# Optimization experiments

Measured on AMD Instinct MI355X. Metric: run time of the kernel, lower is better.

## Reference

```python
import jax, jax.numpy as jnp
import numpy as np

HIDDEN = 7168
N_HEADS = 32
QK_NOPE = 128
QK_ROPE = 64
V_DIM = 128
Q_LORA = 1536
KV_LORA = 512
ROPE_THETA = 10000.0
EPS = 1e-6
T = 2048
W_SCALE = 0.02


def setup_inputs() -> dict:
    key = jax.random.key(0)
    ks = jax.random.split(key, 8)
    return {
        "hidden_states": jax.random.normal(ks[0], (T, HIDDEN), jnp.float32),
        "positions": jnp.arange(T, dtype=jnp.int32),
        "wq_a": jax.random.normal(ks[1], (HIDDEN, Q_LORA), jnp.float32) * W_SCALE,
        "q_a_ln_w": jnp.ones((Q_LORA,), jnp.float32),
        "wq_b": jax.random.normal(ks[2], (Q_LORA, N_HEADS * (QK_NOPE + QK_ROPE)), jnp.float32) * W_SCALE,
        "wkv_a": jax.random.normal(ks[3], (HIDDEN, KV_LORA + QK_ROPE), jnp.float32) * W_SCALE,
        "kv_a_ln_w": jnp.ones((KV_LORA,), jnp.float32),
        "wkv_b": jax.random.normal(ks[4], (KV_LORA, N_HEADS * (QK_NOPE + V_DIM)), jnp.float32) * W_SCALE,
        "wo": jax.random.normal(ks[5], (N_HEADS * V_DIM, HIDDEN), jnp.float32) * W_SCALE,
    }


def _rmsnorm(x, w, eps=EPS):
    var = jnp.mean(jnp.square(x), axis=-1, keepdims=True)
    return x * jax.lax.rsqrt(var + eps) * w


def _rope_cos_sin(positions):
    # deepseek rope: base**(arange(0, d, 2)/d), interleaved (non-neox) layout
    inv_freq = 1.0 / (ROPE_THETA ** (jnp.arange(0, QK_ROPE, 2, dtype=jnp.float32) / QK_ROPE))
    ang = positions.astype(jnp.float32)[:, None] * inv_freq[None, :]  # [T, 32]
    return jnp.cos(ang), jnp.sin(ang)


def _apply_rope_interleaved(x, cos, sin):
    # x: [T, H, QK_ROPE]; even/odd interleaved pairs
    x1 = x[..., 0::2]
    x2 = x[..., 1::2]
    c = cos[:, None, :]
    s = sin[:, None, :]
    o1 = x1 * c - x2 * s
    o2 = x1 * s + x2 * c
    return jnp.stack([o1, o2], axis=-1).reshape(x.shape)


def reference(hidden_states, positions, wq_a, q_a_ln_w, wq_b, wkv_a, kv_a_ln_w, wkv_b, wo):
    scaling = (QK_NOPE + QK_ROPE) ** -0.5
    # q low-rank path: a-proj -> RMSNorm -> b-proj
    q = _rmsnorm(hidden_states @ wq_a, q_a_ln_w) @ wq_b  # [T, H*192]
    q = q.reshape(T, N_HEADS, QK_NOPE + QK_ROPE)
    q_nope, q_rope = q[..., :QK_NOPE], q[..., QK_NOPE:]
    # kv low-rank path
    latent = hidden_states @ wkv_a  # [T, KV_LORA + QK_ROPE]
    c_kv, k_rope = latent[:, :KV_LORA], latent[:, KV_LORA:]
    c_kv = _rmsnorm(c_kv, kv_a_ln_w)
    # decoupled RoPE on q_rope and shared k_rope
    cos, sin = _rope_cos_sin(positions)
    q_rope = _apply_rope_interleaved(q_rope, cos, sin)
    k_rope = _apply_rope_interleaved(k_rope[:, None, :], cos, sin)  # [T,1,64]
    # expand latent to per-head k_nope and v (kv_b_proj)
    kv = (c_kv @ wkv_b).reshape(T, N_HEADS, QK_NOPE + V_DIM)
    k_nope, v = kv[..., :QK_NOPE], kv[..., QK_NOPE:]
    k = jnp.concatenate([k_nope, jnp.broadcast_to(k_rope, (T, N_HEADS, QK_ROPE))], axis=-1)
    qf = jnp.concatenate([q_nope, q_rope], axis=-1)  # [T,H,192]
    # causal MHA
    scores = jnp.einsum("qhd,khd->hqk", qf, k) * scaling
    mask = jnp.tril(jnp.ones((T, T), dtype=bool))
    scores = jnp.where(mask[None], scores, -jnp.inf)
    p = jax.nn.softmax(scores, axis=-1)
    attn = jnp.einsum("hqk,khd->qhd", p, v).reshape(T, N_HEADS * V_DIM)
    return attn @ wo  # [T, HIDDEN]
```

## Files before the change

### kernel.cpp

```cpp
#include <hip/hip_runtime.h>
#include <stdint.h>

#define T_SEQ 2048
#define HID 7168
#define NH 32
#define DN 128
#define DR 64
#define DQK 192
#define DV 128
#define QL 1536
#define KVL 512
#define LATD 576
#define QD 6144
#define KVD 8192
#define WOK 4096
#define NCAT 2112

typedef unsigned short u16;
typedef __bf16 bf16x8 __attribute__((ext_vector_type(8)));
typedef float f32x4 __attribute__((ext_vector_type(4)));

__device__ __forceinline__ u16 f2bf(float f) {
  union { float f; unsigned u; } v; v.f = f;
  unsigned r = v.u + 0x7FFFu + ((v.u >> 16) & 1u);
  return (u16)(r >> 16);
}
__device__ __forceinline__ float bf2f(u16 s) {
  union { unsigned u; float f; } v; v.u = ((unsigned)s) << 16;
  return v.f;
}

__device__ __forceinline__ void gl2lds16(const void* g, void* l) {
  __builtin_amdgcn_global_load_lds((const __attribute__((address_space(1))) void*)g,
                                   (__attribute__((address_space(3))) void*)l, 16, 0, 0);
}

__device__ __forceinline__ f32x4 mfma16(bf16x8 a, bf16x8 b, f32x4 c) {
  return __builtin_amdgcn_mfma_f32_16x16x32_bf16(a, b, c, 0, 0, 0);
}

__device__ __forceinline__ void store_out(float* p, float v) { *p = v; }
__device__ __forceinline__ void store_out(u16* p, float v) { *p = f2bf(v); }

#define FENCE() asm volatile("" ::: "memory")

__global__ __launch_bounds__(256) void k_cvt_bf16(const float* __restrict__ in,
                                                  u16* __restrict__ out, long long n) {
  long long i = ((long long)blockIdx.x * 256 + threadIdx.x) * 8;
  if (i >= n) return;
  const float4* p = (const float4*)(in + i);
  float4 a = p[0], b = p[1];
  union { uint4 v; u16 s[8]; } o;
  o.s[0]=f2bf(a.x); o.s[1]=f2bf(a.y); o.s[2]=f2bf(a.z); o.s[3]=f2bf(a.w);
  o.s[4]=f2bf(b.x); o.s[5]=f2bf(b.y); o.s[6]=f2bf(b.z); o.s[7]=f2bf(b.w);
  *(uint4*)(out + i) = o.v;
}

__global__ __launch_bounds__(256) void k_transpose_bf16(const float* __restrict__ in,
                                                        u16* __restrict__ out, int R, int C,
                                                        float scale) {
  __shared__ float tile[64][65];
  int c0 = blockIdx.x * 64, r0 = blockIdx.y * 64;
  int tx = threadIdx.x & 15, ty = threadIdx.x >> 4;
  #pragma unroll
  for (int i = 0; i < 4; i++) {
    int r = ty + i * 16;
    float4 v = *(const float4*)(in + (size_t)(r0 + r) * C + c0 + tx * 4);
    tile[r][tx*4+0] = v.x; tile[r][tx*4+1] = v.y; tile[r][tx*4+2] = v.z; tile[r][tx*4+3] = v.w;
  }
  __syncthreads();
  #pragma unroll
  for (int i = 0; i < 4; i++) {
    int oc = ty + i * 16;
    union { uint2 v; u16 s[4]; } o;
    #pragma unroll
    for (int j = 0; j < 4; j++) o.s[j] = f2bf(tile[tx*4+j][oc] * scale);
    *(uint2*)(out + (size_t)(c0 + oc) * R + r0 + tx * 4) = o.v;
  }
}

__global__ __launch_bounds__(256) void k_rmsnorm_bf16(const float* __restrict__ x,
                                                      const float* __restrict__ w,
                                                      u16* __restrict__ out, int n, int ldin) {
  int row = blockIdx.x;
  const float* xr = x + (size_t)row * ldin;
  u16* orow = out + (size_t)row * n;
  float ss = 0.f;
  for (int i = threadIdx.x * 4; i < n; i += 1024) {
    float4 v = *(const float4*)(xr + i);
    ss += v.x*v.x + v.y*v.y + v.z*v.z + v.w*v.w;
  }
  #pragma unroll
  for (int off = 32; off > 0; off >>= 1) ss += __shfl_xor(ss, off);
  __shared__ float red[4];
  if ((threadIdx.x & 63) == 0) red[threadIdx.x >> 6] = ss;
  __syncthreads();
  float tot = red[0] + red[1] + red[2] + red[3];
  float rstd = rsqrtf(tot / (float)n + 1e-6f);
  for (int i = threadIdx.x * 4; i < n; i += 1024) {
    float4 v = *(const float4*)(xr + i);
    float4 g = *(const float4*)(w + i);
    union { uint2 u; u16 s[4]; } o;
    o.s[0]=f2bf(v.x*rstd*g.x); o.s[1]=f2bf(v.y*rstd*g.y);
    o.s[2]=f2bf(v.z*rstd*g.z); o.s[3]=f2bf(v.w*rstd*g.w);
    *(uint2*)(orow + i) = o.u;
  }
}

__global__ __launch_bounds__(256) void k_gemm_bt(const u16* __restrict__ A,
                                                 const u16* __restrict__ Bt,
                                                 float* __restrict__ C,
                                                 int M, int N, int K) {
  __shared__ __attribute__((aligned(16))) u16 As[128 * 32];
  __shared__ __attribute__((aligned(16))) u16 Bs[128 * 32];
  int m0 = blockIdx.y * 128, n0 = blockIdx.x * 128;
  int tid = threadIdx.x;
  int w = tid >> 6, lane = tid & 63, l16 = lane & 15, lh = lane >> 4;
  int wr = (w >> 1) * 64, wc = (w & 1) * 64;
  f32x4 zero = {0.f, 0.f, 0.f, 0.f};
  f32x4 acc[4][4];
  #pragma unroll
  for (int i = 0; i < 4; i++)
    #pragma unroll
    for (int j = 0; j < 4; j++) acc[i][j] = zero;
  int ra = tid >> 2, ca = (tid & 3) * 8;
  const u16* a0 = A + (size_t)(m0 + ra) * K + ca;
  const u16* a1 = A + (size_t)(m0 + ra + 64) * K + ca;
  int rb0 = n0 + ra;      rb0 = rb0 < N ? rb0 : N - 1;
  int rb1 = n0 + ra + 64; rb1 = rb1 < N ? rb1 : N - 1;
  const u16* b0 = Bt + (size_t)rb0 * K + ca;
  const u16* b1 = Bt + (size_t)rb1 * K + ca;
  for (int k0 = 0; k0 < K; k0 += 32) {
    gl2lds16(a0 + k0, &As[tid * 8]);
    gl2lds16(a1 + k0, &As[2048 + tid * 8]);
    gl2lds16(b0 + k0, &Bs[tid * 8]);
    gl2lds16(b1 + k0, &Bs[2048 + tid * 8]);
    __syncthreads();
    bf16x8 af[4], bv[4];
    #pragma unroll
    for (int i = 0; i < 4; i++) af[i] = *(const bf16x8*)&As[(wr + i * 16 + l16) * 32 + lh * 8];
    #pragma unroll
    for (int j = 0; j < 4; j++) bv[j] = *(const bf16x8*)&Bs[(wc + j * 16 + l16) * 32 + lh * 8];
    #pragma unroll
    for (int i = 0; i < 4; i++)
      #pragma unroll
      for (int j = 0; j < 4; j++)
        acc[i][j] = mfma16(af[i], bv[j], acc[i][j]);
    __syncthreads();
  }
  #pragma unroll
  for (int i = 0; i < 4; i++) {
    #pragma unroll
    for (int j = 0; j < 4; j++) {
      int col = n0 + wc + j * 16 + l16;
      if (col < N) {
        #pragma unroll
        for (int r = 0; r < 4; r++) {
          int row = m0 + wr + i * 16 + lh * 4 + r;
          C[(size_t)row * N + col] = acc[i][j][r];
        }
      }
    }
  }
}

template <typename OutT>
__global__ __launch_bounds__(512) void k_gemm_bt256(const u16* __restrict__ A,
                                                    const u16* __restrict__ Bt,
                                                    OutT* __restrict__ C,
                                                    int N, int K) {
  __shared__ __attribute__((aligned(16))) u16 lds[3 * 16384];
  const int tid = threadIdx.x;
  const int lane = tid & 63, l16 = lane & 15, lh = lane >> 4;
  const int w = tid >> 6, wm = w >> 2, wn = w & 3;
  const int m0 = blockIdx.y * 256, n0 = blockIdx.x * 256;
  const int nt = K >> 5;

  f32x4 acc[8][4];
  #pragma unroll
  for (int i = 0; i < 8; i++)
    #pragma unroll
    for (int j = 0; j < 4; j++) acc[i][j] = f32x4{0.f, 0.f, 0.f, 0.f};

  const int P = tid * 16;
  const int ls = P ^ (((P >> 7) & 7) << 4);
  const int sr = ls >> 6;
  const int sce = (ls & 63) >> 1;
  const u16* gA0 = A + (size_t)(m0 + sr) * K + sce;
  const u16* gA1 = A + (size_t)(m0 + sr + 128) * K + sce;
  const u16* gB0 = Bt + (size_t)(n0 + sr) * K + sce;
  const u16* gB1 = Bt + (size_t)(n0 + sr + 128) * K + sce;
  u16* ldst = &lds[tid * 8];

  for (int pt = 0; pt < 2 && pt < nt; ++pt) {
    gl2lds16(gA0 + pt * 32, ldst + pt * 16384);
    gl2lds16(gA1 + pt * 32, ldst + pt * 16384 + 4096);
    gl2lds16(gB0 + pt * 32, ldst + pt * 16384 + 8192);
    gl2lds16(gB1 + pt * 32, ldst + pt * 16384 + 12288);
  }
  __syncthreads();

  int bufr = 0;
  for (int t = 0; t < nt; ++t) {
    const bool more = (t + 2) < nt;
    const int bw = (t + 2) % 3;
    const u16* As = &lds[bufr * 16384];
    const u16* Bs = &lds[bufr * 16384 + 8192];
    bf16x8 afr[4], bfr[4];
    #pragma unroll
    for (int j = 0; j < 4; ++j) {
      int L = ((wn * 64 + j * 16 + l16) << 6) + (lh << 4);
      bfr[j] = *(const bf16x8*)((const char*)Bs + (L ^ (((L >> 7) & 7) << 4)));
    }
    #pragma unroll
    for (int i = 0; i < 4; ++i) {
      int L = ((wm * 128 + i * 16 + l16) << 6) + (lh << 4);
      afr[i] = *(const bf16x8*)((const char*)As + (L ^ (((L >> 7) & 7) << 4)));
    }
    if (more) {
      gl2lds16(gA0 + (t + 2) * 32, ldst + bw * 16384);
      gl2lds16(gA1 + (t + 2) * 32, ldst + bw * 16384 + 4096);
    }
    FENCE();
    __builtin_amdgcn_s_barrier();
    FENCE();
    __builtin_amdgcn_s_setprio(1);
    #pragma unroll
    for (int i = 0; i < 4; ++i)
      #pragma unroll
      for (int j = 0; j < 4; ++j)
        acc[i][j] = mfma16(afr[i], bfr[j], acc[i][j]);
    __builtin_amdgcn_s_setprio(0);
    FENCE();
    __builtin_amdgcn_s_barrier();
    FENCE();
    #pragma unroll
    for (int i = 0; i < 4; ++i) {
      int L = ((wm * 128 + 64 + i * 16 + l16) << 6) + (lh << 4);
      afr[i] = *(const bf16x8*)((const char*)As + (L ^ (((L >> 7) & 7) << 4)));
    }
    if (more) {
      gl2lds16(gB0 + (t + 2) * 32, ldst + bw * 16384 + 8192);
      gl2lds16(gB1 + (t + 2) * 32, ldst + bw * 16384 + 12288);
    }
    FENCE();
    __builtin_amdgcn_s_barrier();
    FENCE();
    __builtin_amdgcn_s_setprio(1);
    #pragma unroll
    for (int i = 0; i < 4; ++i)
      #pragma unroll
      for (int j = 0; j < 4; ++j)
        acc[4 + i][j] = mfma16(afr[i], bfr[j], acc[4 + i][j]);
    __builtin_amdgcn_s_setprio(0);
    FENCE();
    if (more) asm volatile("s_waitcnt vmcnt(4)" ::: "memory");
    else      asm volatile("s_waitcnt vmcnt(0)" ::: "memory");
    __builtin_amdgcn_s_barrier();
    FENCE();
    bufr = (bufr == 2) ? 0 : bufr + 1;
  }

  #pragma unroll
  for (int hf = 0; hf < 2; ++hf) {
    #pragma unroll
    for (int i = 0; i < 4; ++i) {
      int rbase = m0 + wm * 128 + hf * 64 + i * 16 + lh * 4;
      #pragma unroll
      for (int j = 0; j < 4; ++j) {
        int col = n0 + wn * 64 + j * 16 + l16;
        #pragma unroll
        for (int r = 0; r < 4; ++r)
          store_out(&C[(size_t)(rbase + r) * N + col], acc[hf * 4 + i][j][r]);
      }
    }
  }
}

__global__ __launch_bounds__(256) void k_build_q(const u16* __restrict__ qf,
                                                 const int* __restrict__ pos,
                                                 u16* __restrict__ Qc) {
  int t = blockIdx.x;
  __shared__ float cs[32], sn[32];
  if (threadIdx.x < 32) {
    float inv = expf(-9.2103403719761836f * (float)threadIdx.x / 32.f);
    float ang = (float)pos[t] * inv;
    cs[threadIdx.x] = cosf(ang);
    sn[threadIdx.x] = sinf(ang);
  }
  __syncthreads();
  const u16* qrow = qf + (size_t)t * QD;
  for (int e = threadIdx.x; e < QD; e += 256) {
    int h = e / 192, d = e - h * 192;
    u16 outv;
    if (d < DN) {
      outv = qrow[e];
    } else {
      int dr = d - DN, i = dr >> 1;
      float x1 = bf2f(qrow[h * 192 + DN + 2 * i]), x2 = bf2f(qrow[h * 192 + DN + 2 * i + 1]);
      float v = (dr & 1) ? (x1 * sn[i] + x2 * cs[i]) : (x1 * cs[i] - x2 * sn[i]);
      outv = f2bf(v);
    }
    Qc[((size_t)h * T_SEQ + t) * DQK + d] = outv;
  }
}

__global__ __launch_bounds__(256) void k_build_k(const u16* __restrict__ kvf,
                                                 const float* __restrict__ kr, int krld,
                                                 const int* __restrict__ pos,
                                                 u16* __restrict__ Kc) {
  int t = blockIdx.x;
  __shared__ u16 kro[64];
  if (threadIdx.x < 32) {
    int i = threadIdx.x;
    float inv = expf(-9.2103403719761836f * (float)i / 32.f);
    float ang = (float)pos[t] * inv;
    float c = cosf(ang), s = sinf(ang);
    float x1 = kr[(size_t)t * krld + 2 * i];
    float x2 = kr[(size_t)t * krld + 2 * i + 1];
    kro[2 * i]     = f2bf(x1 * c - x2 * s);
    kro[2 * i + 1] = f2bf(x1 * s + x2 * c);
  }
  __syncthreads();
  const u16* krow = kvf + (size_t)t * KVD;
  for (int e = threadIdx.x; e < NH * DQK; e += 256) {
    int h = e / 192, d = e - h * 192;
    Kc[((size_t)h * T_SEQ + t) * DQK + d] = (d < DN) ? krow[h * 256 + d] : kro[d - DN];
  }
}

__global__ __launch_bounds__(256) void k_build_vt(const u16* __restrict__ kvf,
                                                  u16* __restrict__ Vt) {
  __shared__ unsigned tile[64][65];
  int t0 = blockIdx.x * 64, d0 = blockIdx.y * 64, h = blockIdx.z;
  int tid = threadIdx.x;
  #pragma unroll
  for (int i = 0; i < 2; i++) {
    int r = (tid >> 3) + i * 32;
    int c = (tid & 7) * 8;
    uint4 v = *(const uint4*)(kvf + (size_t)(t0 + r) * KVD + h * 256 + DN + d0 + c);
    const u16* s = (const u16*)&v;
    #pragma unroll
    for (int j = 0; j < 8; j++) tile[r][c + j] = s[j];
  }
  __syncthreads();
  #pragma unroll
  for (int i = 0; i < 2; i++) {
    int d = (tid >> 3) + i * 32;
    int tb = (tid & 7) * 8;
    union { uint4 v; u16 s[8]; } o;
    #pragma unroll
    for (int j = 0; j < 8; j++) o.s[j] = (u16)tile[tb + j][d];
    *(uint4*)(Vt + ((size_t)h * DV + d0 + d) * T_SEQ + t0 + tb) = o.v;
  }
}

__global__ __launch_bounds__(256) void k_mla_attn(const u16* __restrict__ Qc,
                                                  const u16* __restrict__ Kc,
                                                  const u16* __restrict__ Vt,
                                                  u16* __restrict__ attn) {
  int qt = blockIdx.x, h = blockIdx.y;
  __shared__ __attribute__((aligned(16))) u16 Ks[64 * 192];
  __shared__ __attribute__((aligned(16))) u16 Vs[128 * 64];
  __shared__ __attribute__((aligned(16))) u16 Ps[64 * 64];
  int tid = threadIdx.x, w = tid >> 6, lane = tid & 63, l16 = lane & 15, lh = lane >> 4;
  int swz = (l16 & 7) << 4;

  const char* Qg = (const char*)(Qc + ((size_t)h * T_SEQ + (size_t)qt * 64) * DQK);
  #pragma unroll
  for (int i = 0; i < 6; i++) {
    int L = tid * 16 + i * 4096;
    int row = L / 384;
    gl2lds16(Qg + (L ^ ((row & 7) << 4)), (char*)Ks + L);
  }
  __syncthreads();
  bf16x8 aq[6];
  #pragma unroll
  for (int kf = 0; kf < 6; kf++)
    aq[kf] = *(const bf16x8*)((const char*)Ks + (w * 16 + l16) * 384 + ((kf * 64 + lh * 16) ^ swz));
  __syncthreads();

  f32x4 zero = {0.f, 0.f, 0.f, 0.f};
  f32x4 accO[8];
  #pragma unroll
  for (int i = 0; i < 8; i++) accO[i] = zero;
  float m[4]    = {-3e38f, -3e38f, -3e38f, -3e38f};
  float lsum[4] = {0.f, 0.f, 0.f, 0.f};

  const char* Kb = (const char*)(Kc + (size_t)h * T_SEQ * DQK);
  const char* Vb = (const char*)(Vt + (size_t)h * DV * T_SEQ);

  for (int kt = 0; kt <= qt; ++kt) {
    const char* Kg = Kb + (size_t)kt * 64 * DQK * 2;
    #pragma unroll
    for (int i = 0; i < 6; i++) {
      int L = tid * 16 + i * 4096;
      int row = L / 384;
      gl2lds16(Kg + (L ^ ((row & 7) << 4)), (char*)Ks + L);
    }
    #pragma unroll
    for (int i = 0; i < 4; i++) {
      int L = tid * 16 + i * 4096;
      int row = L >> 7, wb = L & 127;
      gl2lds16(Vb + (size_t)row * (T_SEQ * 2) + (size_t)kt * 128 + (wb ^ ((row & 7) << 4)),
               (char*)Vs + L);
    }
    __syncthreads();

    f32x4 sf[4];
    #pragma unroll
    for (int j = 0; j < 4; j++) sf[j] = zero;
    #pragma unroll
    for (int kf = 0; kf < 6; ++kf) {
      #pragma unroll
      for (int j = 0; j < 4; ++j) {
        bf16x8 bk = *(const bf16x8*)((const char*)Ks + (j * 16 + l16) * 384 +
                                     ((kf * 64 + lh * 16) ^ swz));
        sf[j] = mfma16(aq[kf], bk, sf[j]);
      }
    }
    bool diag = (kt == qt);
    #pragma unroll
    for (int rr = 0; rr < 4; ++rr) {
      int qrow = qt * 64 + w * 16 + lh * 4 + rr;
      float rowm = -3e38f;
      #pragma unroll
      for (int j = 0; j < 4; ++j) {
        float s = sf[j][rr];
        if (diag && (kt * 64 + j * 16 + l16) > qrow) s = -3e38f;
        sf[j][rr] = s;
        rowm = fmaxf(rowm, s);
      }
      rowm = fmaxf(rowm, __shfl_xor(rowm, 1));
      rowm = fmaxf(rowm, __shfl_xor(rowm, 2));
      rowm = fmaxf(rowm, __shfl_xor(rowm, 4));
      rowm = fmaxf(rowm, __shfl_xor(rowm, 8));
      float mnew = fmaxf(m[rr], rowm);
      float sc = __expf(m[rr] - mnew);
      float pj[4];
      float ps = 0.f;
      #pragma unroll
      for (int j = 0; j < 4; ++j) { pj[j] = __expf(sf[j][rr] - mnew); ps += pj[j]; }
      ps += __shfl_xor(ps, 1); ps += __shfl_xor(ps, 2);
      ps += __shfl_xor(ps, 4); ps += __shfl_xor(ps, 8);
      lsum[rr] = lsum[rr] * sc + ps;
      m[rr] = mnew;
      #pragma unroll
      for (int of = 0; of < 8; ++of) accO[of][rr] *= sc;
      int r = w * 16 + lh * 4 + rr;
      int rsw = (r & 7) << 4;
      #pragma unroll
      for (int j = 0; j < 4; ++j)
        *(u16*)((char*)Ps + r * 128 + ((2 * (j * 16 + l16)) ^ rsw)) = f2bf(pj[j]);
    }
    #pragma unroll
    for (int kf = 0; kf < 2; ++kf) {
      bf16x8 ap = *(const bf16x8*)((const char*)Ps + (w * 16 + l16) * 128 +
                                   ((kf * 64 + lh * 16) ^ swz));
      #pragma unroll
      for (int of = 0; of < 8; ++of) {
        bf16x8 bvv = *(const bf16x8*)((const char*)Vs + (of * 16 + l16) * 128 +
                                      ((kf * 64 + lh * 16) ^ swz));
        accO[of] = mfma16(ap, bvv, accO[of]);
      }
    }
    __syncthreads();
  }
  #pragma unroll
  for (int rr = 0; rr < 4; ++rr) {
    float inv = 1.f / lsum[rr];
    int t = qt * 64 + w * 16 + lh * 4 + rr;
    #pragma unroll
    for (int of = 0; of < 8; ++of)
      attn[(size_t)t * WOK + h * DV + of * 16 + l16] = f2bf(accO[of][rr] * inv);
  }
}

extern "C" void kernel_launch(void* const* d_in, const int* in_sizes, int n_in,
                              void* d_out, int out_size, void* d_ws, size_t ws_size,
                              hipStream_t stream) {
  const float* hidden     = (const float*)d_in[0];
  const int*   positions  = (const int*)d_in[1];
  const float* wq_a       = (const float*)d_in[2];
  const float* q_a_ln_w   = (const float*)d_in[3];
  const float* wq_b       = (const float*)d_in[4];
  const float* wkv_a      = (const float*)d_in[5];
  const float* kv_a_ln_w  = (const float*)d_in[6];
  const float* wkv_b      = (const float*)d_in[7];
  const float* wo         = (const float*)d_in[8];
  float* out = (float*)d_out;

  char* p = (char*)d_ws;
  size_t off = 0;
  auto alloc = [&](size_t bytes) -> void* {
    void* r = p + off;
    off += (bytes + 255) & ~(size_t)255;
    return r;
  };
  u16*   h_bf = (u16*)  alloc((size_t)T_SEQ * HID * 2);
  u16*   wbuf = (u16*)  alloc((size_t)HID * WOK * 2);
  u16*   bigh = (u16*)  alloc((size_t)T_SEQ * KVD * 2);
  float* cat  = (float*)alloc((size_t)T_SEQ * NCAT * 4);
  u16*   qln  = (u16*)  alloc((size_t)T_SEQ * QL * 2);
  u16*   ckv  = (u16*)  alloc((size_t)T_SEQ * KVL * 2);
  u16*   Qc   = (u16*)  alloc((size_t)NH * T_SEQ * DQK * 2);
  u16*   Kc   = (u16*)  alloc((size_t)NH * T_SEQ * DQK * 2);
  u16*   Vt   = (u16*)  alloc((size_t)NH * DV * T_SEQ * 2);
  u16*   attn = (u16*)  alloc((size_t)T_SEQ * WOK * 2);

  k_cvt_bf16<<<(T_SEQ * HID) / (256 * 8), 256, 0, stream>>>(hidden, h_bf, (long long)T_SEQ * HID);

  k_transpose_bf16<<<dim3(QL / 64, HID / 64), 256, 0, stream>>>(wq_a, wbuf, HID, QL, 1.0f);
  k_transpose_bf16<<<dim3(LATD / 64, HID / 64), 256, 0, stream>>>(wkv_a, wbuf + (size_t)QL * HID,
                                                                  HID, LATD, 1.0f);
  k_gemm_bt<<<dim3((NCAT + 127) / 128, T_SEQ / 128), 256, 0, stream>>>(h_bf, wbuf, cat,
                                                                       T_SEQ, NCAT, HID);

  k_rmsnorm_bf16<<<T_SEQ, 256, 0, stream>>>(cat + QL, kv_a_ln_w, ckv, KVL, NCAT);
  k_transpose_bf16<<<dim3(KVD / 64, KVL / 64), 256, 0, stream>>>(wkv_b, wbuf, KVL, KVD, 1.0f);
  k_gemm_bt256<u16><<<dim3(KVD / 256, T_SEQ / 256), 512, 0, stream>>>(ckv, wbuf, bigh, KVD, KVL);
  k_build_k<<<T_SEQ, 256, 0, stream>>>(bigh, cat + QL + KVL, NCAT, positions, Kc);
  k_build_vt<<<dim3(T_SEQ / 64, 2, NH), 256, 0, stream>>>(bigh, Vt);

  k_rmsnorm_bf16<<<T_SEQ, 256, 0, stream>>>(cat, q_a_ln_w, qln, QL, NCAT);
  k_transpose_bf16<<<dim3(QD / 64, QL / 64), 256, 0, stream>>>(wq_b, wbuf, QL, QD,
                                                               0.07216878364870322f);
  k_gemm_bt256<u16><<<dim3(QD / 256, T_SEQ / 256), 512, 0, stream>>>(qln, wbuf, bigh, QD, QL);
  k_build_q<<<T_SEQ, 256, 0, stream>>>(bigh, positions, Qc);

  k_mla_attn<<<dim3(T_SEQ / 64, NH), 256, 0, stream>>>(Qc, Kc, Vt, attn);

  k_transpose_bf16<<<dim3(HID / 64, WOK / 64), 256, 0, stream>>>(wo, wbuf, WOK, HID, 1.0f);
  k_gemm_bt256<float><<<dim3(HID / 256, T_SEQ / 256), 512, 0, stream>>>(attn, wbuf, out, HID, WOK);
}
```

Before: 676.1 us.

## Double-buffer K tiles, read V into registers, schedule heaviest query tiles first

The attention kernel now prefetches the next K tile into a second LDS buffer while the current tile is being computed, instead of loading and then waiting at a barrier. V fragments are loaded straight from global memory into registers for each tile, so the V shared-memory buffer is gone. The grid is flattened so the largest causal query tiles start first, and launch bounds request two blocks per CU. The aim is to hide load latency and balance the causal workload, at the cost of more registers and V reads that now depend on L2 hit rates.

```diff
diff --git a/kernel.cpp b/kernel.cpp
--- a/kernel.cpp
+++ b/kernel.cpp
@@ -355,16 +355,21 @@
   }
 }
 
-__global__ __launch_bounds__(256) void k_mla_attn(const u16* __restrict__ Qc,
-                                                  const u16* __restrict__ Kc,
-                                                  const u16* __restrict__ Vt,
-                                                  u16* __restrict__ attn) {
-  int qt = blockIdx.x, h = blockIdx.y;
-  __shared__ __attribute__((aligned(16))) u16 Ks[64 * 192];
-  __shared__ __attribute__((aligned(16))) u16 Vs[128 * 64];
+__global__ __launch_bounds__(256, 2) void k_mla_attn(const u16* __restrict__ Qc,
+                                                     const u16* __restrict__ Kc,
+                                                     const u16* __restrict__ Vt,
+                                                     u16* __restrict__ attn) {
+  __shared__ __attribute__((aligned(16))) u16 Ks[2 * 64 * 192];
   __shared__ __attribute__((aligned(16))) u16 Ps[64 * 64];
+  int bid = blockIdx.x;
+  int hi = bid >> 8, r = bid & 255;
+  int qt = 31 - (r >> 3);
+  int h = (hi << 3) | (r & 7);
   int tid = threadIdx.x, w = tid >> 6, lane = tid & 63, l16 = lane & 15, lh = lane >> 4;
   int swz = (l16 & 7) << 4;
+
+  const char* Kb = (const char*)(Kc + (size_t)h * T_SEQ * DQK);
+  const u16* Vh = Vt + (size_t)h * DV * T_SEQ;
 
   const char* Qg = (const char*)(Qc + ((size_t)h * T_SEQ + (size_t)qt * 64) * DQK);
   #pragma unroll
@@ -373,6 +378,12 @@
     int row = L / 384;
     gl2lds16(Qg + (L ^ ((row & 7) << 4)), (char*)Ks + L);
   }
+  #pragma unroll
+  for (int i = 0; i < 6; i++) {
+    int L = tid * 16 + i * 4096;
+    int row = L / 384;
+    gl2lds16(Kb + (L ^ ((row & 7) << 4)), (char*)Ks + 24576 + L);
+  }
   __syncthreads();
   bf16x8 aq[6];
   #pragma unroll
@@ -387,25 +398,25 @@
   float m[4]    = {-3e38f, -3e38f, -3e38f, -3e38f};
   float lsum[4] = {0.f, 0.f, 0.f, 0.f};
 
-  const char* Kb = (const char*)(Kc + (size_t)h * T_SEQ * DQK);
-  const char* Vb = (const char*)(Vt + (size_t)h * DV * T_SEQ);
-
   for (int kt = 0; kt <= qt; ++kt) {
-    const char* Kg = Kb + (size_t)kt * 64 * DQK * 2;
-    #pragma unroll
-    for (int i = 0; i < 6; i++) {
-      int L = tid * 16 + i * 4096;
-      int row = L / 384;
-      gl2lds16(Kg + (L ^ ((row & 7) << 4)), (char*)Ks + L);
-    }
-    #pragma unroll
-    for (int i = 0; i < 4; i++) {
-      int L = tid * 16 + i * 4096;
-      int row = L >> 7, wb = L & 127;
-      gl2lds16(Vb + (size_t)row * (T_SEQ * 2) + (size_t)kt * 128 + (wb ^ ((row & 7) << 4)),
-               (char*)Vs + L);
-    }
-    __syncthreads();
+    const char* Kcur = (const char*)Ks + (1 - (kt & 1)) * 24576;
+    char* Kstg = (char*)Ks + (kt & 1) * 24576;
+    if (kt < qt) {
+      const char* Kg = Kb + (size_t)(kt + 1) * 64 * DQK * 2;
+      #pragma unroll
+      for (int i = 0; i < 6; i++) {
+        int L = tid * 16 + i * 4096;
+        int row = L / 384;
+        gl2lds16(Kg + (L ^ ((row & 7) << 4)), Kstg + L);
+      }
+    }
+    bf16x8 vf[16];
+    #pragma unroll
+    for (int of = 0; of < 8; ++of)
+      #pragma unroll
+      for (int kf = 0; kf < 2; ++kf)
+        vf[of * 2 + kf] = *(const bf16x8*)(Vh + (size_t)(of * 16 + l16) * T_SEQ +
+                                           kt * 64 + kf * 32 + lh * 8);
 
     f32x4 sf[4];
     #pragma unroll
@@ -414,8 +425,7 @@
     for (int kf = 0; kf < 6; ++kf) {
       #pragma unroll
       for (int j = 0; j < 4; ++j) {
-        bf16x8 bk = *(const bf16x8*)((const char*)Ks + (j * 16 + l16) * 384 +
-                                     ((kf * 64 + lh * 16) ^ swz));
+        bf16x8 bk = *(const bf16x8*)(Kcur + (j * 16 + l16) * 384 + ((kf * 64 + lh * 16) ^ swz));
         sf[j] = mfma16(aq[kf], bk, sf[j]);
       }
     }
@@ -447,22 +457,19 @@
       m[rr] = mnew;
       #pragma unroll
       for (int of = 0; of < 8; ++of) accO[of][rr] *= sc;
-      int r = w * 16 + lh * 4 + rr;
-      int rsw = (r & 7) << 4;
+      int rw = w * 16 + lh * 4 + rr;
+      int rsw = (rw & 7) << 4;
       #pragma unroll
       for (int j = 0; j < 4; ++j)
-        *(u16*)((char*)Ps + r * 128 + ((2 * (j * 16 + l16)) ^ rsw)) = f2bf(pj[j]);
+        *(u16*)((char*)Ps + rw * 128 + ((2 * (j * 16 + l16)) ^ rsw)) = f2bf(pj[j]);
     }
     #pragma unroll
     for (int kf = 0; kf < 2; ++kf) {
       bf16x8 ap = *(const bf16x8*)((const char*)Ps + (w * 16 + l16) * 128 +
                                    ((kf * 64 + lh * 16) ^ swz));
       #pragma unroll
-      for (int of = 0; of < 8; ++of) {
-        bf16x8 bvv = *(const bf16x8*)((const char*)Vs + (of * 16 + l16) * 128 +
-                                      ((kf * 64 + lh * 16) ^ swz));
-        accO[of] = mfma16(ap, bvv, accO[of]);
-      }
+      for (int of = 0; of < 8; ++of)
+        accO[of] = mfma16(ap, vf[of * 2 + kf], accO[of]);
     }
     __syncthreads();
   }
@@ -528,7 +535,7 @@
   k_gemm_bt256<u16><<<dim3(QD / 256, T_SEQ / 256), 512, 0, stream>>>(qln, wbuf, bigh, QD, QL);
   k_build_q<<<T_SEQ, 256, 0, stream>>>(bigh, positions, Qc);
 
-  k_mla_attn<<<dim3(T_SEQ / 64, NH), 256, 0, stream>>>(Qc, Kc, Vt, attn);
+  k_mla_attn<<<1024, 256, 0, stream>>>(Qc, Kc, Vt, attn);
 
   k_transpose_bf16<<<dim3(HID / 64, WOK / 64), 256, 0, stream>>>(wo, wbuf, WOK, HID, 1.0f);
   k_gemm_bt256<float><<<dim3(HID / 256, T_SEQ / 256), 512, 0, stream>>>(attn, wbuf, out, HID, WOK);
```

New measurement: 684.1 us. No clear change (+1.2%).
